# Optimization experiments

Measured on AMD Instinct MI355X. Metric: run time of the kernel, lower is better.

## Reference

```python
import jax, jax.numpy as jnp
import numpy as np

N = 100000          # nodes
E = 1_600_000       # edges (before self-loops)
F_IN = 128          # input node features
H1, C1 = 8, 16      # layer-1 heads / per-head channels (concat -> 128)
NUM_CLASSES = 40
NEG_SLOPE = 0.2


def _gat_conv(x, src, dst, W, a_src, a_dst, b, concat):
    """PyG-style GATConv (eval mode, self-loops already in src/dst)."""
    n = x.shape[0]
    H, C = a_src.shape
    h = (x @ W).reshape(n, H, C)                      # [N,H,C]
    s_src = jnp.einsum('nhc,hc->nh', h, a_src)        # [N,H] per-node src logits
    s_dst = jnp.einsum('nhc,hc->nh', h, a_dst)        # [N,H] per-node dst logits
    e = jax.nn.leaky_relu(s_src[src] + s_dst[dst], NEG_SLOPE)   # [E',H]
    # segment softmax over destination node
    m = jax.ops.segment_max(e, dst, num_segments=n)   # [N,H]
    m = jnp.where(jnp.isfinite(m), m, jnp.zeros_like(m))
    p = jnp.exp(e - m[dst])                           # [E',H]
    denom = jax.ops.segment_sum(p, dst, num_segments=n)
    alpha = p / (denom[dst] + 1e-16)                  # [E',H]
    out = jax.ops.segment_sum(alpha[:, :, None] * h[src], dst, num_segments=n)  # [N,H,C]
    out = out.reshape(n, H * C) if concat else out.mean(axis=1)
    return out + b


def setup_inputs() -> dict:
    key = jax.random.key(0)
    ks = jax.random.split(key, 10)
    glorot = lambda k, shp: jax.random.normal(k, shp, jnp.float32) * np.sqrt(2.0 / (shp[0] + shp[-1] if len(shp) > 1 else shp[0]))
    return {
        'x': jax.random.normal(ks[0], (N, F_IN), jnp.float32),
        'edge_index': jax.random.randint(ks[1], (2, E), 0, N, jnp.int64),
        'W1': glorot(ks[2], (F_IN, H1 * C1)),
        'att_src1': glorot(ks[3], (H1, C1)),
        'att_dst1': glorot(ks[4], (H1, C1)),
        'b1': jnp.zeros((H1 * C1,), jnp.float32),
        'W2': glorot(ks[5], (H1 * C1, NUM_CLASSES)),
        'att_src2': glorot(ks[6], (1, NUM_CLASSES)),
        'att_dst2': glorot(ks[7], (1, NUM_CLASSES)),
        'b2': jnp.zeros((NUM_CLASSES,), jnp.float32),
    }


def reference(x, edge_index, W1, att_src1, att_dst1, b1, W2, att_src2, att_dst2, b2):
    n = x.shape[0]
    loops = jnp.arange(n, dtype=edge_index.dtype)
    src = jnp.concatenate([edge_index[0], loops])     # add self-loops (PyG default)
    dst = jnp.concatenate([edge_index[1], loops])
    h = _gat_conv(x, src, dst, W1, att_src1, att_dst1, b1, concat=True)   # [N,128]
    h = jax.nn.relu(h)
    # dropout: identity in eval mode
    out = _gat_conv(h, src, dst, W2, att_src2, att_dst2, b2, concat=True) # heads=1 -> [N,40]
    return jax.nn.log_softmax(out, axis=1)
```

## Files before the change

kernel.cpp:

```cpp
#include <hip/hip_runtime.h>
#include <math.h>

#define N_NODES 100000
#define F_IN    128
#define H1      8
#define C1      16
#define D1      128
#define NCLS    40
#define NEG     0.2f

typedef unsigned int uint32;
typedef unsigned short ushort16;
typedef float v2f __attribute__((ext_vector_type(2)));

__device__ __forceinline__ ushort16 f2bf(float f) {
    unsigned int u = __float_as_uint(f);
    u += 0x7fffu + ((u >> 16) & 1u);
    return (ushort16)(u >> 16);
}
__device__ __forceinline__ float bf_lo(uint32 p) { return __uint_as_float(p << 16); }
__device__ __forceinline__ float bf_hi(uint32 p) { return __uint_as_float(p & 0xffff0000u); }

__global__ __launch_bounds__(256) void gemm1_kernel(
    const float* __restrict__ x, const float* __restrict__ W,
    uint32* __restrict__ h8,
    const float* __restrict__ a_src, const float* __restrict__ a_dst,
    float* __restrict__ ssrc, float* __restrict__ sdst)
{
    __shared__ float xs[64][132];
    __shared__ float wt[128][68];
    const int row0 = blockIdx.x * 64;
    const int tid = threadIdx.x;
#pragma unroll
    for (int i = 0; i < 8; ++i) {
        int idx = tid + i * 256;
        int r = idx >> 5, c4 = idx & 31;
        float4 v = make_float4(0.f, 0.f, 0.f, 0.f);
        if (row0 + r < N_NODES)
            v = ((const float4*)x)[(size_t)(row0 + r) * 32 + c4];
        *(float4*)&xs[r][c4 * 4] = v;
    }
    const int cg = tid & 15;
    const int rg = tid >> 4;
    float acc[4][8];
#pragma unroll
    for (int i = 0; i < 4; ++i)
#pragma unroll
        for (int j = 0; j < 8; ++j) acc[i][j] = 0.f;

    const int stc = tid & 127;
    const int sth = tid >> 7;
#pragma unroll
    for (int chunk = 0; chunk < 2; ++chunk) {
        const int kbase = chunk * 64;
        __syncthreads();
#pragma unroll
        for (int kk = 0; kk < 8; ++kk) {
            int k = sth * 32 + kk * 4;
            float4 v;
            v.x = W[(size_t)(kbase + k)     * 128 + stc];
            v.y = W[(size_t)(kbase + k + 1) * 128 + stc];
            v.z = W[(size_t)(kbase + k + 2) * 128 + stc];
            v.w = W[(size_t)(kbase + k + 3) * 128 + stc];
            *(float4*)&wt[stc][k] = v;
        }
        __syncthreads();
        for (int k0 = 0; k0 < 64; k0 += 4) {
            float4 wa[8];
#pragma unroll
            for (int j = 0; j < 8; ++j)
                wa[j] = *(const float4*)&wt[cg + 16 * j][k0];
#pragma unroll
            for (int i = 0; i < 4; ++i) {
                float4 hx = *(const float4*)&xs[rg + 16 * i][kbase + k0];
#pragma unroll
                for (int j = 0; j < 8; ++j) {
                    acc[i][j] = fmaf(hx.x, wa[j].x, acc[i][j]);
                    acc[i][j] = fmaf(hx.y, wa[j].y, acc[i][j]);
                    acc[i][j] = fmaf(hx.z, wa[j].z, acc[i][j]);
                    acc[i][j] = fmaf(hx.w, wa[j].w, acc[i][j]);
                }
            }
        }
    }
    __syncthreads();
#pragma unroll
    for (int i = 0; i < 4; ++i)
#pragma unroll
        for (int j = 0; j < 8; ++j)
            xs[rg + 16 * i][cg + 16 * j] = acc[i][j];
    __syncthreads();
#pragma unroll
    for (int t = 0; t < 4; ++t) {
        int task = tid + t * 256;
        int r = task >> 4, g = task & 15;
        if (row0 + r < N_NODES) {
            float4 a = *(const float4*)&xs[r][8 * g];
            float4 b = *(const float4*)&xs[r][8 * g + 4];
            int p0 = __builtin_amdgcn_cvt_pk_fp8_f32(a.x, a.y, 0, false);
            p0     = __builtin_amdgcn_cvt_pk_fp8_f32(a.z, a.w, p0, true);
            int p1 = __builtin_amdgcn_cvt_pk_fp8_f32(b.x, b.y, 0, false);
            p1     = __builtin_amdgcn_cvt_pk_fp8_f32(b.z, b.w, p1, true);
            uint2 pk; pk.x = (uint32)p0; pk.y = (uint32)p1;
            ((uint2*)h8)[(size_t)(row0 + r) * 16 + g] = pk;
        }
    }
#pragma unroll
    for (int t = 0; t < 2; ++t) {
        int task = tid + t * 256;
        int r = task >> 3, hh = task & 7;
        if (row0 + r < N_NODES) {
            float as = 0.f, ad = 0.f;
#pragma unroll
            for (int c = 0; c < 16; ++c) {
                float v = xs[r][hh * 16 + c];
                as = fmaf(v, a_src[hh * 16 + c], as);
                ad = fmaf(v, a_dst[hh * 16 + c], ad);
            }
            ssrc[(row0 + r) * 8 + hh] = as;
            sdst[(row0 + r) * 8 + hh] = ad;
        }
    }
}

__global__ void count_kernel(const int* __restrict__ ei, int E,
                             int* __restrict__ deg,
                             int* __restrict__ rank)
{
    int e = blockIdx.x * blockDim.x + threadIdx.x;
    if (e < E) rank[e] = atomicAdd(&deg[ei[E + e]], 1);
}

__global__ void scan1_kernel(const int* __restrict__ deg,
                             int* __restrict__ incl,
                             int* __restrict__ bsum)
{
    __shared__ int tmp[256];
    int i = blockIdx.x * 256 + threadIdx.x;
    int v = (i < N_NODES) ? deg[i] : 0;
    tmp[threadIdx.x] = v;
    __syncthreads();
    for (int o = 1; o < 256; o <<= 1) {
        int t = (threadIdx.x >= (unsigned)o) ? tmp[threadIdx.x - o] : 0;
        __syncthreads();
        tmp[threadIdx.x] += t;
        __syncthreads();
    }
    if (i < N_NODES) incl[i] = tmp[threadIdx.x];
    if (threadIdx.x == 255) bsum[blockIdx.x] = tmp[255];
}

__global__ void scan2_kernel(int* __restrict__ bsum, int nb)
{
    __shared__ int tmp[512];
    int v = (threadIdx.x < (unsigned)nb) ? bsum[threadIdx.x] : 0;
    tmp[threadIdx.x] = v;
    __syncthreads();
    for (int o = 1; o < 512; o <<= 1) {
        int t = (threadIdx.x >= (unsigned)o) ? tmp[threadIdx.x - o] : 0;
        __syncthreads();
        tmp[threadIdx.x] += t;
        __syncthreads();
    }
    if (threadIdx.x < (unsigned)nb) bsum[threadIdx.x] = tmp[threadIdx.x] - v;
}

__global__ void scan3_kernel(const int* __restrict__ incl,
                             const int* __restrict__ bsum,
                             int* __restrict__ offsets)
{
    int i = blockIdx.x * 256 + threadIdx.x;
    if (i < N_NODES) offsets[i + 1] = incl[i] + bsum[blockIdx.x];
    if (i == 0) offsets[0] = 0;
}

__global__ void scatter_kernel(const int* __restrict__ ei, int E,
                               const int* __restrict__ offsets,
                               const int* __restrict__ rank,
                               int* __restrict__ srcs)
{
    int e = blockIdx.x * blockDim.x + threadIdx.x;
    if (e >= E) return;
    int s = ei[e], d = ei[E + e];
    srcs[offsets[d] + rank[e]] = s;
}

__global__ void gather1_kernel(const uint32* __restrict__ h8,
                               const float* __restrict__ ssrc,
                               const float* __restrict__ sdst,
                               const int* __restrict__ offsets,
                               const int* __restrict__ srcs,
                               const float* __restrict__ b1,
                               float* __restrict__ out)
{
    int d = (blockIdx.x * blockDim.x + threadIdx.x) >> 6;
    int lane = threadIdx.x & 63;
    if (d >= N_NODES) return;
    const int hw = lane & 7;
    const int half = lane >> 5;
    const int u = lane & 31;
    const int hc = u >> 2;
    const float sd_w = sdst[d * H1 + hw];

    float acc0 = 0.f, acc1 = 0.f, acc2 = 0.f, acc3 = 0.f;
    float wsum = 0.f;

    float lgs = ssrc[d * H1 + hc] + sdst[d * H1 + hc];
    lgs = lgs >= 0.f ? lgs : NEG * lgs;
    const float ws_self = __expf(lgs);
    {
        float m = (half == 0) ? ws_self : 0.f;
        uint32 p = h8[(size_t)d * 32 + u];
        v2f lo = __builtin_amdgcn_cvt_pk_f32_fp8((int)p, false);
        v2f hi = __builtin_amdgcn_cvt_pk_f32_fp8((int)p, true);
        acc0 = m * lo[0]; acc1 = m * lo[1];
        acc2 = m * hi[0]; acc3 = m * hi[1];
    }

    const int beg = offsets[d], end = offsets[d + 1];
    int base = beg;
    for (; base + 8 <= end; base += 8) {
        int s_l = srcs[base + (lane >> 3)];
        float lg = ssrc[s_l * H1 + hw] + sd_w;
        lg = lg >= 0.f ? lg : NEG * lg;
        float w_l = __expf(lg);
        wsum += w_l;
#pragma unroll
        for (int t = 0; t < 4; ++t) {
            int j = 2 * t + half;
            int s = __shfl(s_l, j << 3);
            float w = __shfl(w_l, (j << 3) | hc);
            uint32 p = h8[(size_t)s * 32 + u];
            v2f lo = __builtin_amdgcn_cvt_pk_f32_fp8((int)p, false);
            v2f hi = __builtin_amdgcn_cvt_pk_f32_fp8((int)p, true);
            acc0 = fmaf(w, lo[0], acc0);
            acc1 = fmaf(w, lo[1], acc1);
            acc2 = fmaf(w, hi[0], acc2);
            acc3 = fmaf(w, hi[1], acc3);
        }
    }
    int cnt = end - base;
    if (cnt > 0) {
        int s_l = 0; float w_l = 0.f;
        if ((lane >> 3) < cnt) {
            s_l = srcs[base + (lane >> 3)];
            float lg = ssrc[s_l * H1 + hw] + sd_w;
            lg = lg >= 0.f ? lg : NEG * lg;
            w_l = __expf(lg);
        }
        wsum += w_l;
        int steps = (cnt + 1) >> 1;
        for (int t = 0; t < steps; ++t) {
            int j = 2 * t + half;
            int s = __shfl(s_l, j << 3);
            float w = __shfl(w_l, (j << 3) | hc);
            uint32 p = h8[(size_t)s * 32 + u];
            v2f lo = __builtin_amdgcn_cvt_pk_f32_fp8((int)p, false);
            v2f hi = __builtin_amdgcn_cvt_pk_f32_fp8((int)p, true);
            acc0 = fmaf(w, lo[0], acc0);
            acc1 = fmaf(w, lo[1], acc1);
            acc2 = fmaf(w, hi[0], acc2);
            acc3 = fmaf(w, hi[1], acc3);
        }
    }
    wsum += __shfl_xor(wsum, 8);
    wsum += __shfl_xor(wsum, 16);
    wsum += __shfl_xor(wsum, 32);
    float ws = ws_self + __shfl(wsum, hc);
    acc0 += __shfl_xor(acc0, 32);
    acc1 += __shfl_xor(acc1, 32);
    acc2 += __shfl_xor(acc2, 32);
    acc3 += __shfl_xor(acc3, 32);
    if (half == 0) {
        float inv = 1.f / (ws + 1e-16f);
        float4 bb = ((const float4*)b1)[u];
        float4 r;
        r.x = fmaf(acc0, inv, bb.x); r.x = r.x > 0.f ? r.x : 0.f;
        r.y = fmaf(acc1, inv, bb.y); r.y = r.y > 0.f ? r.y : 0.f;
        r.z = fmaf(acc2, inv, bb.z); r.z = r.z > 0.f ? r.z : 0.f;
        r.w = fmaf(acc3, inv, bb.w); r.w = r.w > 0.f ? r.w : 0.f;
        ((float4*)(out + (size_t)d * D1))[u] = r;
    }
}

__global__ __launch_bounds__(256) void gemm2_kernel(
    const float* __restrict__ h, const float* __restrict__ W2,
    ushort16* __restrict__ h2b,
    const float* __restrict__ a_src, const float* __restrict__ a_dst,
    float* __restrict__ ssrc, float* __restrict__ sdst)
{
    __shared__ float w2s[40][132];
    __shared__ float hs[32][132];
    const int row0 = blockIdx.x * 32;
    const int tid = threadIdx.x;
#pragma unroll
    for (int i = 0; i < 20; ++i) {
        int idx = tid + i * 256;
        int k = idx / 40, c = idx % 40;
        w2s[c][k] = W2[idx];
    }
#pragma unroll
    for (int i = 0; i < 4; ++i) {
        int idx = tid + i * 256;
        int r = idx >> 5, c4 = idx & 31;
        *(float4*)&hs[r][c4 * 4] = ((const float4*)h)[(size_t)(row0 + r) * 32 + c4];
    }
    __syncthreads();
    const int rg = tid >> 3;
    const int g  = tid & 7;
    float acc[5] = {0.f, 0.f, 0.f, 0.f, 0.f};
    for (int k0 = 0; k0 < 128; k0 += 4) {
        float4 hv = *(const float4*)&hs[rg][k0];
#pragma unroll
        for (int j = 0; j < 5; ++j) {
            float4 wv = *(const float4*)&w2s[5 * g + j][k0];
            acc[j] = fmaf(hv.x, wv.x, acc[j]);
            acc[j] = fmaf(hv.y, wv.y, acc[j]);
            acc[j] = fmaf(hv.z, wv.z, acc[j]);
            acc[j] = fmaf(hv.w, wv.w, acc[j]);
        }
    }
#pragma unroll
    for (int j = 0; j < 5; ++j)
        h2b[(size_t)(row0 + rg) * 40 + 5 * g + j] = f2bf(acc[j]);
    __syncthreads();
#pragma unroll
    for (int j = 0; j < 5; ++j)
        hs[rg][5 * g + j] = acc[j];
    __syncthreads();
    if (tid < 32) {
        float as = 0.f, ad = 0.f;
#pragma unroll
        for (int c = 0; c < 40; ++c) {
            float v = hs[tid][c];
            as = fmaf(v, a_src[c], as);
            ad = fmaf(v, a_dst[c], ad);
        }
        ssrc[row0 + tid] = as;
        sdst[row0 + tid] = ad;
    }
}

__global__ void gather2_kernel(const uint32* __restrict__ h2b,
                               const float* __restrict__ ssrc,
                               const float* __restrict__ sdst,
                               const int* __restrict__ offsets,
                               const int* __restrict__ srcs,
                               const float* __restrict__ b2,
                               float* __restrict__ out)
{
    int d = (blockIdx.x * blockDim.x + threadIdx.x) >> 6;
    int lane = threadIdx.x & 63;
    if (d >= N_NODES) return;
    const float sd = sdst[d];
    const int g = lane / 20;
    const int c = lane - 20 * g;
    const bool act = lane < (NCLS / 2);
    float acc0 = 0.f, acc1 = 0.f, ws = 0.f;

    {
        float lg = ssrc[d] + sd; lg = lg >= 0.f ? lg : NEG * lg;
        float w = __expf(lg);
        uint32 p = act ? h2b[(size_t)d * 20 + lane] : 0u;
        float m = act ? w : 0.f;
        acc0 = m * bf_lo(p); acc1 = m * bf_hi(p);
        ws = w;
    }
    const int beg = offsets[d], end = offsets[d + 1];
    for (int base = beg; base < end; base += 64) {
        int cnt = end - base; if (cnt > 64) cnt = 64;
        int s_l = 0; float w_l = 0.f;
        if (lane < cnt) {
            s_l = srcs[base + lane];
            float lg = ssrc[s_l] + sd; lg = lg >= 0.f ? lg : NEG * lg;
            w_l = __expf(lg);
        }
        float t = w_l;
#pragma unroll
        for (int o = 32; o > 0; o >>= 1) t += __shfl_xor(t, o);
        ws += t;
        for (int j = 0; j < cnt; j += 3) {
            int jj = j + g;
            int s = __shfl(s_l, jj & 63);
            float w = __shfl(w_l, jj & 63);
            if (g >= 3 || jj >= cnt) w = 0.f;
            uint32 p = h2b[(size_t)s * 20 + c];
            acc0 = fmaf(w, bf_lo(p), acc0);
            acc1 = fmaf(w, bf_hi(p), acc1);
        }
    }
    float r00 = __shfl(acc0, lane + 20), r01 = __shfl(acc0, lane + 40);
    float r10 = __shfl(acc1, lane + 20), r11 = __shfl(acc1, lane + 40);
    float l0 = -INFINITY, l1 = -INFINITY;
    if (act) {
        acc0 += r00 + r01;
        acc1 += r10 + r11;
        float inv = 1.f / (ws + 1e-16f);
        l0 = fmaf(acc0, inv, b2[2 * lane]);
        l1 = fmaf(acc1, inv, b2[2 * lane + 1]);
    }
    float m = fmaxf(l0, l1);
#pragma unroll
    for (int o = 32; o > 0; o >>= 1) m = fmaxf(m, __shfl_xor(m, o));
    float ex = act ? (__expf(l0 - m) + __expf(l1 - m)) : 0.f;
#pragma unroll
    for (int o = 32; o > 0; o >>= 1) ex += __shfl_xor(ex, o);
    float lse = __logf(ex) + m;
    if (act) {
        float2 r; r.x = l0 - lse; r.y = l1 - lse;
        ((float2*)(out + (size_t)d * NCLS))[lane] = r;
    }
}

extern "C" void kernel_launch(void* const* d_in, const int* in_sizes, int n_in,
                              void* d_out, int out_size, void* d_ws, size_t ws_size,
                              hipStream_t stream)
{
    const float* x   = (const float*)d_in[0];
    const int*   ei  = (const int*)  d_in[1];
    const float* W1  = (const float*)d_in[2];
    const float* as1 = (const float*)d_in[3];
    const float* ad1 = (const float*)d_in[4];
    const float* b1  = (const float*)d_in[5];
    const float* W2  = (const float*)d_in[6];
    const float* as2 = (const float*)d_in[7];
    const float* ad2 = (const float*)d_in[8];
    const float* b2  = (const float*)d_in[9];
    float* out = (float*)d_out;
    const int E = in_sizes[1] / 2;

    float* ws = (float*)d_ws;
    size_t off = 0;
    uint32* h1f8 = (uint32*)(ws + off); off += (size_t)N_NODES * 32;
    float* h1r  = ws + off; off += (size_t)N_NODES * D1;
    float* ss1  = ws + off; off += (size_t)N_NODES * H1;
    float* sd1  = ws + off; off += (size_t)N_NODES * H1;
    uint32* h2b = (uint32*)(ws + off); off += (size_t)N_NODES * 20;
    float* ss2  = ws + off; off += N_NODES;
    float* sd2  = ws + off; off += N_NODES;
    int* ib = (int*)(ws + off);
    size_t ioff = 0;
    int* deg     = ib + ioff; ioff += N_NODES;
    int* incl    = ib + ioff; ioff += N_NODES;
    int* offsets = ib + ioff; ioff += N_NODES + 1;
    int* bsum    = ib + ioff; ioff += 512;
    int* rank    = ib + ioff; ioff += E;
    int* srcs    = ib + ioff; ioff += E;

    hipMemsetAsync(deg, 0, (size_t)N_NODES * sizeof(int), stream);

    const int nb = (N_NODES + 255) / 256;
    count_kernel<<<(E + 255) / 256, 256, 0, stream>>>(ei, E, deg, rank);
    scan1_kernel<<<nb, 256, 0, stream>>>(deg, incl, bsum);
    scan2_kernel<<<1, 512, 0, stream>>>(bsum, nb);
    scan3_kernel<<<nb, 256, 0, stream>>>(incl, bsum, offsets);
    scatter_kernel<<<(E + 255) / 256, 256, 0, stream>>>(ei, E, offsets, rank, srcs);

    gemm1_kernel<<<(N_NODES + 63) / 64, 256, 0, stream>>>(x, W1, h1f8, as1, ad1, ss1, sd1);
    gather1_kernel<<<(N_NODES * 64 + 255) / 256, 256, 0, stream>>>(h1f8, ss1, sd1, offsets, srcs, b1, h1r);

    gemm2_kernel<<<N_NODES / 32, 256, 0, stream>>>(h1r, W2, (ushort16*)h2b, as2, ad2, ss2, sd2);
    gather2_kernel<<<(N_NODES * 64 + 255) / 256, 256, 0, stream>>>(h2b, ss2, sd2, offsets, srcs, b2, out);
}
```

Baseline: 414.8 us.

## Fuse edge degree counting into gemm1 launch and double gemm2 rows per block

```diff
diff --git a/kernel.cpp b/kernel.cpp
--- a/kernel.cpp
+++ b/kernel.cpp
@@ -21,16 +21,30 @@
 __device__ __forceinline__ float bf_lo(uint32 p) { return __uint_as_float(p << 16); }
 __device__ __forceinline__ float bf_hi(uint32 p) { return __uint_as_float(p & 0xffff0000u); }
 
-__global__ __launch_bounds__(256) void gemm1_kernel(
+#define NG 1563
+
+__global__ __launch_bounds__(256) void gemm1_count_kernel(
     const float* __restrict__ x, const float* __restrict__ W,
     uint32* __restrict__ h8,
     const float* __restrict__ a_src, const float* __restrict__ a_dst,
-    float* __restrict__ ssrc, float* __restrict__ sdst)
+    float* __restrict__ ssrc, float* __restrict__ sdst,
+    const int* __restrict__ ei, int E,
+    int* __restrict__ deg, int* __restrict__ rank)
 {
     __shared__ float xs[64][132];
     __shared__ float wt[128][68];
-    const int row0 = blockIdx.x * 64;
+    const int bid = blockIdx.x;
     const int tid = threadIdx.x;
+    const bool is_gemm = ((bid % 5) == 0) && (bid / 5 < NG);
+    if (!is_gemm) {
+        int ng_before = bid / 5 + ((bid % 5) ? 1 : 0);
+        if (ng_before > NG) ng_before = NG;
+        int c = bid - ng_before;
+        long long e = (long long)c * 256 + tid;
+        if (e < E) rank[e] = atomicAdd(&deg[ei[E + e]], 1);
+        return;
+    }
+    const int row0 = (bid / 5) * 64;
 #pragma unroll
     for (int i = 0; i < 8; ++i) {
         int idx = tid + i * 256;
@@ -121,14 +135,6 @@
             sdst[(row0 + r) * 8 + hh] = ad;
         }
     }
-}
-
-__global__ void count_kernel(const int* __restrict__ ei, int E,
-                             int* __restrict__ deg,
-                             int* __restrict__ rank)
-{
-    int e = blockIdx.x * blockDim.x + threadIdx.x;
-    if (e < E) rank[e] = atomicAdd(&deg[ei[E + e]], 1);
 }
 
 __global__ void scan1_kernel(const int* __restrict__ deg,
@@ -290,8 +296,8 @@
     float* __restrict__ ssrc, float* __restrict__ sdst)
 {
     __shared__ float w2s[40][132];
-    __shared__ float hs[32][132];
-    const int row0 = blockIdx.x * 32;
+    __shared__ float hs[64][132];
+    const int row0 = blockIdx.x * 64;
     const int tid = threadIdx.x;
 #pragma unroll
     for (int i = 0; i < 20; ++i) {
@@ -300,35 +306,55 @@
         w2s[c][k] = W2[idx];
     }
 #pragma unroll
-    for (int i = 0; i < 4; ++i) {
+    for (int i = 0; i < 8; ++i) {
         int idx = tid + i * 256;
         int r = idx >> 5, c4 = idx & 31;
-        *(float4*)&hs[r][c4 * 4] = ((const float4*)h)[(size_t)(row0 + r) * 32 + c4];
-    }
-    __syncthreads();
-    const int rg = tid >> 3;
+        float4 v = make_float4(0.f, 0.f, 0.f, 0.f);
+        if (row0 + r < N_NODES)
+            v = ((const float4*)h)[(size_t)(row0 + r) * 32 + c4];
+        *(float4*)&hs[r][c4 * 4] = v;
+    }
+    __syncthreads();
+    const int rr = tid >> 3;
     const int g  = tid & 7;
-    float acc[5] = {0.f, 0.f, 0.f, 0.f, 0.f};
+    float acc[2][5];
+#pragma unroll
+    for (int t = 0; t < 2; ++t)
+#pragma unroll
+        for (int j = 0; j < 5; ++j) acc[t][j] = 0.f;
     for (int k0 = 0; k0 < 128; k0 += 4) {
-        float4 hv = *(const float4*)&hs[rg][k0];
+        float4 ha = *(const float4*)&hs[rr][k0];
+        float4 hb = *(const float4*)&hs[rr + 32][k0];
 #pragma unroll
         for (int j = 0; j < 5; ++j) {
             float4 wv = *(const float4*)&w2s[5 * g + j][k0];
-            acc[j] = fmaf(hv.x, wv.x, acc[j]);
-            acc[j] = fmaf(hv.y, wv.y, acc[j]);
-            acc[j] = fmaf(hv.z, wv.z, acc[j]);
-            acc[j] = fmaf(hv.w, wv.w, acc[j]);
-        }
-    }
-#pragma unroll
-    for (int j = 0; j < 5; ++j)
-        h2b[(size_t)(row0 + rg) * 40 + 5 * g + j] = f2bf(acc[j]);
-    __syncthreads();
-#pragma unroll
-    for (int j = 0; j < 5; ++j)
-        hs[rg][5 * g + j] = acc[j];
-    __syncthreads();
-    if (tid < 32) {
+            acc[0][j] = fmaf(ha.x, wv.x, acc[0][j]);
+            acc[0][j] = fmaf(ha.y, wv.y, acc[0][j]);
+            acc[0][j] = fmaf(ha.z, wv.z, acc[0][j]);
+            acc[0][j] = fmaf(ha.w, wv.w, acc[0][j]);
+            acc[1][j] = fmaf(hb.x, wv.x, acc[1][j]);
+            acc[1][j] = fmaf(hb.y, wv.y, acc[1][j]);
+            acc[1][j] = fmaf(hb.z, wv.z, acc[1][j]);
+            acc[1][j] = fmaf(hb.w, wv.w, acc[1][j]);
+        }
+    }
+#pragma unroll
+    for (int t = 0; t < 2; ++t) {
+        int row = row0 + rr + 32 * t;
+        if (row < N_NODES) {
+#pragma unroll
+            for (int j = 0; j < 5; ++j)
+                h2b[(size_t)row * 40 + 5 * g + j] = f2bf(acc[t][j]);
+        }
+    }
+    __syncthreads();
+#pragma unroll
+    for (int t = 0; t < 2; ++t)
+#pragma unroll
+        for (int j = 0; j < 5; ++j)
+            hs[rr + 32 * t][5 * g + j] = acc[t][j];
+    __syncthreads();
+    if (tid < 64 && row0 + tid < N_NODES) {
         float as = 0.f, ad = 0.f;
 #pragma unroll
         for (int c = 0; c < 40; ++c) {
@@ -450,15 +476,17 @@
     hipMemsetAsync(deg, 0, (size_t)N_NODES * sizeof(int), stream);
 
     const int nb = (N_NODES + 255) / 256;
-    count_kernel<<<(E + 255) / 256, 256, 0, stream>>>(ei, E, deg, rank);
+    const int nc = (E + 255) / 256;
+
+    gemm1_count_kernel<<<NG + nc, 256, 0, stream>>>(x, W1, h1f8, as1, ad1,
+                                                    ss1, sd1, ei, E, deg, rank);
     scan1_kernel<<<nb, 256, 0, stream>>>(deg, incl, bsum);
     scan2_kernel<<<1, 512, 0, stream>>>(bsum, nb);
     scan3_kernel<<<nb, 256, 0, stream>>>(incl, bsum, offsets);
     scatter_kernel<<<(E + 255) / 256, 256, 0, stream>>>(ei, E, offsets, rank, srcs);
 
-    gemm1_kernel<<<(N_NODES + 63) / 64, 256, 0, stream>>>(x, W1, h1f8, as1, ad1, ss1, sd1);
     gather1_kernel<<<(N_NODES * 64 + 255) / 256, 256, 0, stream>>>(h1f8, ss1, sd1, offsets, srcs, b1, h1r);
 
-    gemm2_kernel<<<N_NODES / 32, 256, 0, stream>>>(h1r, W2, (ushort16*)h2b, as2, ad2, ss2, sd2);
+    gemm2_kernel<<<(N_NODES + 63) / 64, 256, 0, stream>>>(h1r, W2, (ushort16*)h2b, as2, ad2, ss2, sd2);
     gather2_kernel<<<(N_NODES * 64 + 255) / 256, 256, 0, stream>>>(h2b, ss2, sd2, offsets, srcs, b2, out);
 }
```

Measured after the change: 386.7 us. -6.8%, faster.
